# Kernel optimization log

Hardware: AMD Instinct MI355X
Metric: run time of the kernel (lower is better)

Reference implementation:

```python
import jax, jax.numpy as jnp
import numpy as np

N, M, E, DIM, H = 50000, 50000, 640000, 128, 8
DH = DIM // H
EPS = 1e-5

def _prelu(x, alpha):
    return jnp.where(x >= 0, x, alpha * x)

def setup_inputs() -> dict:
    key0 = jax.random.key(0)
    ks = jax.random.split(key0, 12)
    s = 1.0 / np.sqrt(DIM)
    return {
        "query": jax.random.normal(ks[0], (N, DIM), jnp.float32),
        "key": jax.random.normal(ks[1], (M, DIM), jnp.float32),
        "value": jax.random.normal(ks[2], (M, DIM), jnp.float32),
        "query_idx": jax.random.randint(ks[3], (E,), 0, N),
        "key_idx": jax.random.randint(ks[4], (E,), 0, M),
        "Wq": jax.random.normal(ks[5], (DIM, DIM), jnp.float32) * s,
        "bq": jnp.zeros((DIM,), jnp.float32),
        "Wk": jax.random.normal(ks[6], (DIM, DIM), jnp.float32) * s,
        "bk": jnp.zeros((DIM,), jnp.float32),
        "Wv": jax.random.normal(ks[7], (DIM, DIM), jnp.float32) * s,
        "bv": jnp.zeros((DIM,), jnp.float32),
        "Wp": jax.random.normal(ks[8], (DIM, DIM), jnp.float32) * s,
        "bp": jnp.zeros((DIM,), jnp.float32),
        "a": jax.random.normal(ks[9], (1, H, DH), jnp.float32) * 0.1,
        "alpha": jnp.full((1,), 0.25, jnp.float32),
        "gamma": jnp.ones((DIM,), jnp.float32),
        "beta": jnp.zeros((DIM,), jnp.float32),
    }

def reference(query, key, value, query_idx, key_idx, Wq, bq, Wk, bk, Wv, bv, Wp, bp, a, alpha, gamma, beta):
    n = query.shape[0]
    # projections (node-level, then gather per edge; linear commutes with gather)
    Qq = query @ Wq + bq            # [N, DIM]
    Kq = query @ Wk + bk            # [N, DIM] (self-attn key)
    Kk = key @ Wk + bk              # [M, DIM]
    Vq = query @ Wv + bv            # [N, DIM]
    Vv = value @ Wv + bv            # [M, DIM]
    # self-attention score per query node: [N, H, 1]
    attn_qq = (a * _prelu(Qq + Kq, alpha).reshape(n, H, DH)).sum(-1, keepdims=True)
    # per-edge additive attention score: [E, H, 1]
    e_feat = _prelu(Qq[query_idx] + Kk[key_idx], alpha)
    attn_e = (a * e_feat.reshape(-1, H, DH)).sum(-1, keepdims=True)
    # stable softmax over irregular query groups (include self)
    max_attn = jax.lax.stop_gradient(attn_qq.at[query_idx].max(attn_e))
    exp_qq = jnp.exp(attn_qq - max_attn)                 # [N, H, 1]
    exp_e = jnp.exp(attn_e - max_attn[query_idx])        # [E, H, 1]
    denom = exp_qq.at[query_idx].add(exp_e)              # [N, H, 1]
    denom = jnp.where(denom == 0, 1.0, denom)
    # weighted value scatter-sum (value_idx == key_idx)
    msg = exp_qq * Vq.reshape(n, H, DH)
    msg = msg.at[query_idx].add(exp_e * Vv[key_idx].reshape(-1, H, DH))
    out = (msg / denom).reshape(n, DIM) @ Wp + bp
    res = query + out
    mu = res.mean(-1, keepdims=True)
    var = res.var(-1, keepdims=True)
    return gamma * (res - mu) / jnp.sqrt(var + EPS) + beta
```

## Files before the change

kernel.cpp:

```cpp
#include <hip/hip_runtime.h>
#include <math.h>

#define DIM 128
#define NH 8
#define LN_EPS 1e-5f
#define NEGINF -3.0e38f

using bf16x8 = __attribute__((ext_vector_type(8))) short;
using f32x4  = __attribute__((ext_vector_type(4))) float;

__device__ __forceinline__ float prelu_f(float x, float al) { return x >= 0.f ? x : al * x; }

__device__ __forceinline__ short f2bf(float f) {
    unsigned u = __float_as_uint(f);
    unsigned r = (u + 0x7fffu + ((u >> 16) & 1u)) >> 16;
    return (short)r;
}
__device__ __forceinline__ float bflo(unsigned u) { return __uint_as_float(u << 16); }
__device__ __forceinline__ float bfhi(unsigned u) { return __uint_as_float(u & 0xffff0000u); }

__device__ __forceinline__ unsigned cvt_pk_bf16(float lo, float hi) {
    unsigned r;
    asm("v_cvt_pk_bf16_f32 %0, %1, %2" : "=v"(r) : "v"(lo), "v"(hi));
    return r;
}

__device__ __forceinline__ float swz_xor1(float x) {
    return __int_as_float(__builtin_amdgcn_ds_swizzle(__float_as_int(x), 0x041F));
}
__device__ __forceinline__ float swz_xor2(float x) {
    return __int_as_float(__builtin_amdgcn_ds_swizzle(__float_as_int(x), 0x081F));
}
__device__ __forceinline__ float swz_xor4(float x) {
    return __int_as_float(__builtin_amdgcn_ds_swizzle(__float_as_int(x), 0x101F));
}
__device__ __forceinline__ float swz_xor8(float x) {
    return __int_as_float(__builtin_amdgcn_ds_swizzle(__float_as_int(x), 0x201F));
}
__device__ __forceinline__ float swz_xor16(float x) {
    return __int_as_float(__builtin_amdgcn_ds_swizzle(__float_as_int(x), 0x401F));
}
__device__ __forceinline__ float swz_xor32(float x) {
    return __shfl_xor(x, 32);
}

__global__ __launch_bounds__(256) void setup_kernel(
    const float* __restrict__ W0, const float* __restrict__ W1,
    const float* __restrict__ W2, const float* __restrict__ W3,
    short* __restrict__ P0, short* __restrict__ P1,
    short* __restrict__ P2, short* __restrict__ P3,
    const int* __restrict__ qidx, int* __restrict__ counts, int E)
{
    if (blockIdx.x < 32) {
        const int id = blockIdx.x * 256 + threadIdx.x;
        const int mat = id >> 11;
        const int rem = id & 2047;
        const int ks = rem >> 9;
        const int ct = (rem >> 6) & 7;
        const int lane = rem & 63;
        const int lr = lane & 15, lg = lane >> 4;
        const float* W = mat == 0 ? W0 : mat == 1 ? W1 : mat == 2 ? W2 : W3;
        short* P = mat == 0 ? P0 : mat == 1 ? P1 : mat == 2 ? P2 : P3;
        short v[8];
        #pragma unroll
        for (int r = 0; r < 8; ++r)
            v[r] = f2bf(W[(ks * 32 + lg * 8 + r) * DIM + ct * 16 + lr]);
        *(bf16x8*)&P[(size_t)((ks * 8 + ct) * 64 + lane) * 8] = *(bf16x8*)v;
    } else {
        const int b = blockIdx.x - 32;
        for (int e = b * 256 + threadIdx.x; e < E; e += 1024 * 256)
            atomicAdd(&counts[qidx[e]], 1);
    }
}

__global__ __launch_bounds__(256) void proj_all_mfma(
    const float* __restrict__ query,
    const float* __restrict__ key, const float* __restrict__ value,
    const short* __restrict__ Wqp, const short* __restrict__ Wkp, const short* __restrict__ Wvp,
    const float* __restrict__ bq, const float* __restrict__ bk, const float* __restrict__ bv,
    const float* __restrict__ avec, const float* __restrict__ alpha_p,
    short* __restrict__ QV16, float* __restrict__ attnqq,
    short* __restrict__ KV16, int N, int M, int nb)
{
    __shared__ unsigned lds[4][16][66];
    const int wid = threadIdx.x >> 6, lane = threadIdx.x & 63;
    const int lr = lane & 15, lg = lane >> 4;
    const bool evenlane = (lane & 1) == 0;

    if ((int)blockIdx.x < nb) {
        const int row0 = ((int)blockIdx.x * 4 + wid) * 16;
        if (row0 >= N) return;
        const int arow = row0 + lr;
        const bool rowok = arow < N;

        bf16x8 afrag[4];
        #pragma unroll
        for (int ks = 0; ks < 4; ++ks) {
            float t[8] = {0.f,0.f,0.f,0.f,0.f,0.f,0.f,0.f};
            if (rowok) {
                *(float4*)&t[0] = *(const float4*)&query[(size_t)arow * DIM + ks * 32 + lg * 8];
                *(float4*)&t[4] = *(const float4*)&query[(size_t)arow * DIM + ks * 32 + lg * 8 + 4];
            }
            union { bf16x8 v; unsigned u[4]; } a;
            a.u[0] = cvt_pk_bf16(t[0], t[1]);
            a.u[1] = cvt_pk_bf16(t[2], t[3]);
            a.u[2] = cvt_pk_bf16(t[4], t[5]);
            a.u[3] = cvt_pk_bf16(t[6], t[7]);
            afrag[ks] = a.v;
        }
        const float al = alpha_p[0];
        unsigned* qvout = (unsigned*)QV16;

        #pragma unroll 1
        for (int ct = 0; ct < 8; ++ct) {
            f32x4 aq = (f32x4)0.f, ak = (f32x4)0.f;
            #pragma unroll
            for (int ks = 0; ks < 4; ++ks) {
                const size_t bo = (size_t)((ks * 8 + ct) * 64 + lane) * 8;
                aq = __builtin_amdgcn_mfma_f32_16x16x32_bf16(afrag[ks], *(const bf16x8*)&Wqp[bo], aq, 0, 0, 0);
                ak = __builtin_amdgcn_mfma_f32_16x16x32_bf16(afrag[ks], *(const bf16x8*)&Wkp[bo], ak, 0, 0, 0);
            }
            const int col = ct * 16 + lr;
            const float bqv = bq[col], bkv = bk[col], av = avec[col];
            #pragma unroll
            for (int r = 0; r < 4; ++r) {
                const int row = lg * 4 + r;
                const float qv = aq[r] + bqv;
                const float kv = ak[r] + bkv;
                float part = av * prelu_f(qv + kv, al);
                part += swz_xor1(part);
                part += swz_xor2(part);
                part += swz_xor4(part);
                part += swz_xor8(part);
                const int grow = row0 + row;
                if (lr == 0 && grow < N) attnqq[(size_t)grow * NH + ct] = part;
                const float qn = swz_xor1(qv);
                if (evenlane) lds[wid][row][ct * 8 + (lr >> 1)] = cvt_pk_bf16(qv, qn);
            }
        }
        #pragma unroll
        for (int rr = 0; rr < 16; ++rr) {
            const int grow = row0 + rr;
            if (grow < N) qvout[(size_t)grow * 128 + lane] = lds[wid][rr][lane];
        }

        #pragma unroll 1
        for (int ct = 0; ct < 8; ++ct) {
            f32x4 acv = (f32x4)0.f;
            #pragma unroll
            for (int ks = 0; ks < 4; ++ks) {
                const size_t bo = (size_t)((ks * 8 + ct) * 64 + lane) * 8;
                acv = __builtin_amdgcn_mfma_f32_16x16x32_bf16(afrag[ks], *(const bf16x8*)&Wvp[bo], acv, 0, 0, 0);
            }
            const int col = ct * 16 + lr;
            const float bvv = bv[col];
            #pragma unroll
            for (int r = 0; r < 4; ++r) {
                const int row = lg * 4 + r;
                const float vv = acv[r] + bvv;
                const float vn = swz_xor1(vv);
                if (evenlane) lds[wid][row][ct * 8 + (lr >> 1)] = cvt_pk_bf16(vv, vn);
            }
        }
        #pragma unroll
        for (int rr = 0; rr < 16; ++rr) {
            const int grow = row0 + rr;
            if (grow < N) qvout[(size_t)grow * 128 + 64 + lane] = lds[wid][rr][lane];
        }
    } else {
        const int row0 = (((int)blockIdx.x - nb) * 4 + wid) * 16;
        if (row0 >= M) return;
        const int arow = row0 + lr;
        const bool rowok = arow < M;
        unsigned* kvout = (unsigned*)KV16;

        {
            bf16x8 afK[4];
            #pragma unroll
            for (int ks = 0; ks < 4; ++ks) {
                float t[8] = {0.f,0.f,0.f,0.f,0.f,0.f,0.f,0.f};
                if (rowok) {
                    *(float4*)&t[0] = *(const float4*)&key[(size_t)arow * DIM + ks * 32 + lg * 8];
                    *(float4*)&t[4] = *(const float4*)&key[(size_t)arow * DIM + ks * 32 + lg * 8 + 4];
                }
                union { bf16x8 v; unsigned u[4]; } a;
                a.u[0] = cvt_pk_bf16(t[0], t[1]);
                a.u[1] = cvt_pk_bf16(t[2], t[3]);
                a.u[2] = cvt_pk_bf16(t[4], t[5]);
                a.u[3] = cvt_pk_bf16(t[6], t[7]);
                afK[ks] = a.v;
            }
            #pragma unroll 1
            for (int ct = 0; ct < 8; ++ct) {
                f32x4 ack = (f32x4)0.f;
                #pragma unroll
                for (int ks = 0; ks < 4; ++ks) {
                    const size_t bo = (size_t)((ks * 8 + ct) * 64 + lane) * 8;
                    ack = __builtin_amdgcn_mfma_f32_16x16x32_bf16(afK[ks], *(const bf16x8*)&Wkp[bo], ack, 0, 0, 0);
                }
                const int col = ct * 16 + lr;
                const float bkv = bk[col];
                #pragma unroll
                for (int r = 0; r < 4; ++r) {
                    const int row = lg * 4 + r;
                    const float kv = ack[r] + bkv;
                    const float kn = swz_xor1(kv);
                    if (evenlane) lds[wid][row][ct * 8 + (lr >> 1)] = cvt_pk_bf16(kv, kn);
                }
            }
            #pragma unroll
            for (int rr = 0; rr < 16; ++rr) {
                const int grow = row0 + rr;
                if (grow < M) kvout[(size_t)grow * 128 + lane] = lds[wid][rr][lane];
            }
        }
        {
            bf16x8 afV[4];
            #pragma unroll
            for (int ks = 0; ks < 4; ++ks) {
                float t[8] = {0.f,0.f,0.f,0.f,0.f,0.f,0.f,0.f};
                if (rowok) {
                    *(float4*)&t[0] = *(const float4*)&value[(size_t)arow * DIM + ks * 32 + lg * 8];
                    *(float4*)&t[4] = *(const float4*)&value[(size_t)arow * DIM + ks * 32 + lg * 8 + 4];
                }
                union { bf16x8 v; unsigned u[4]; } a;
                a.u[0] = cvt_pk_bf16(t[0], t[1]);
                a.u[1] = cvt_pk_bf16(t[2], t[3]);
                a.u[2] = cvt_pk_bf16(t[4], t[5]);
                a.u[3] = cvt_pk_bf16(t[6], t[7]);
                afV[ks] = a.v;
            }
            #pragma unroll 1
            for (int ct = 0; ct < 8; ++ct) {
                f32x4 acv = (f32x4)0.f;
                #pragma unroll
                for (int ks = 0; ks < 4; ++ks) {
                    const size_t bo = (size_t)((ks * 8 + ct) * 64 + lane) * 8;
                    acv = __builtin_amdgcn_mfma_f32_16x16x32_bf16(afV[ks], *(const bf16x8*)&Wvp[bo], acv, 0, 0, 0);
                }
                const int col = ct * 16 + lr;
                const float bvv = bv[col];
                #pragma unroll
                for (int r = 0; r < 4; ++r) {
                    const int row = lg * 4 + r;
                    const float vv = acv[r] + bvv;
                    const float vn = swz_xor1(vv);
                    if (evenlane) lds[wid][row][ct * 8 + (lr >> 1)] = cvt_pk_bf16(vv, vn);
                }
            }
            #pragma unroll
            for (int rr = 0; rr < 16; ++rr) {
                const int grow = row0 + rr;
                if (grow < M) kvout[(size_t)grow * 128 + 64 + lane] = lds[wid][rr][lane];
            }
        }
    }
}

__global__ __launch_bounds__(256) void scan1_kernel(const int* __restrict__ counts,
                                                    int* __restrict__ bsum, int N)
{
    __shared__ int sh[256];
    int i = blockIdx.x * 256 + threadIdx.x;
    sh[threadIdx.x] = (i < N) ? counts[i] : 0;
    __syncthreads();
    #pragma unroll
    for (int off = 128; off; off >>= 1) {
        if (threadIdx.x < off) sh[threadIdx.x] += sh[threadIdx.x + off];
        __syncthreads();
    }
    if (threadIdx.x == 0) bsum[blockIdx.x] = sh[0];
}

__global__ __launch_bounds__(256) void scan2_kernel(const int* __restrict__ bsum,
                                                    int* __restrict__ boff, int B)
{
    int t = threadIdx.x;
    if (B > 256) {
        if (t == 0) { int run = 0; for (int i = 0; i < B; ++i) { int v = bsum[i]; boff[i] = run; run += v; } }
        return;
    }
    __shared__ int sh[256];
    int v = (t < B) ? bsum[t] : 0;
    sh[t] = v;
    __syncthreads();
    for (int off = 1; off < 256; off <<= 1) {
        int x = (t >= off) ? sh[t - off] : 0;
        __syncthreads();
        sh[t] += x;
        __syncthreads();
    }
    if (t < B) boff[t] = sh[t] - v;
}

__global__ __launch_bounds__(256) void scan3_kernel(const int* __restrict__ counts,
                                                    const int* __restrict__ boff,
                                                    int* __restrict__ offsets,
                                                    int* __restrict__ cursor,
                                                    int N, int E)
{
    __shared__ int sh[256];
    int t = threadIdx.x;
    int i = blockIdx.x * 256 + t;
    int v = (i < N) ? counts[i] : 0;
    sh[t] = v;
    __syncthreads();
    for (int off = 1; off < 256; off <<= 1) {
        int x = (t >= off) ? sh[t - off] : 0;
        __syncthreads();
        sh[t] += x;
        __syncthreads();
    }
    int base = boff[blockIdx.x];
    if (i < N) {
        int o = base + sh[t] - v;
        offsets[i] = o;
        cursor[i] = o;
    }
    if (i == 0) offsets[N] = E;
}

__global__ void fill_kernel(const int* __restrict__ qidx, const int* __restrict__ kidx,
                            int* __restrict__ cursor, int* __restrict__ ksorted, int E)
{
    for (int e = blockIdx.x * blockDim.x + threadIdx.x; e < E; e += gridDim.x * blockDim.x) {
        int q = qidx[e];
        int pos = atomicAdd(&cursor[q], 1);
        ksorted[pos] = kidx[e];
    }
}

__global__ __launch_bounds__(256) void edge_agg_kernel(
    const short* __restrict__ QV16, const float* __restrict__ attnqq,
    const short* __restrict__ KV16,
    const int* __restrict__ ksorted, const int* __restrict__ offsets,
    const float* __restrict__ avec, const float* __restrict__ alpha_p,
    short* __restrict__ msgn16, int N)
{
    const int wid = threadIdx.x >> 6;
    const int lane = threadIdx.x & 63;
    const int n = blockIdx.x * 4 + wid;
    if (n >= N) return;

    const int h = lane & 7;
    const int e = lane >> 3;
    const float al = alpha_p[0];

    float c1[16], c2[16];
    {
        const float s1 = (1.f + al) * 0.5f, s2 = (1.f - al) * 0.5f;
        #pragma unroll
        for (int j = 0; j < 4; ++j) {
            const float4 a4 = *(const float4*)&avec[h * 16 + j * 4];
            c1[j*4+0] = a4.x * s1; c2[j*4+0] = a4.x * s2;
            c1[j*4+1] = a4.y * s1; c2[j*4+1] = a4.y * s2;
            c1[j*4+2] = a4.z * s1; c2[j*4+2] = a4.z * s2;
            c1[j*4+3] = a4.w * s1; c2[j*4+3] = a4.w * s2;
        }
    }

    const size_t qb = (size_t)n * 256 + h * 16;
    float q[16];
    {
        const uint4 lo = *(const uint4*)&QV16[qb];
        const uint4 hi = *(const uint4*)&QV16[qb + 8];
        const unsigned qd[8] = {lo.x, lo.y, lo.z, lo.w, hi.x, hi.y, hi.z, hi.w};
        #pragma unroll
        for (int j = 0; j < 8; ++j) { q[2*j] = bflo(qd[j]); q[2*j+1] = bfhi(qd[j]); }
    }

    float acc[16];
    float den;
    if (e == 0) {
        const uint4 lo = *(const uint4*)&QV16[qb + 128];
        const uint4 hi = *(const uint4*)&QV16[qb + 136];
        const unsigned vd[8] = {lo.x, lo.y, lo.z, lo.w, hi.x, hi.y, hi.z, hi.w};
        #pragma unroll
        for (int j = 0; j < 8; ++j) { acc[2*j] = bflo(vd[j]); acc[2*j+1] = bfhi(vd[j]); }
        den = 1.f;
    } else {
        #pragma unroll
        for (int d = 0; d < 16; ++d) acc[d] = 0.f;
        den = 0.f;
    }

    float m = attnqq[(size_t)n * NH + h];
    const int p0 = offsets[n], p1 = offsets[n + 1];
    bool div = false;

    int idx = p0 + e;
    bool valid = idx < p1;
    int ki = valid ? ksorted[idx] : 0;

    for (int base = p0; base < p1; base += 8) {
        const int cki = ki;
        const bool cval = valid;
        const int nidx = base + 8 + e;
        valid = nidx < p1;
        ki = valid ? ksorted[nidx] : 0;

        const size_t kb = (size_t)cki * 256 + h * 16;
        const uint4 klo = *(const uint4*)&KV16[kb];
        const uint4 khi = *(const uint4*)&KV16[kb + 8];
        const uint4 vlo = *(const uint4*)&KV16[kb + 128];
        const uint4 vhi = *(const uint4*)&KV16[kb + 136];
        const unsigned kd[8] = {klo.x, klo.y, klo.z, klo.w, khi.x, khi.y, khi.z, khi.w};
        const unsigned vd[8] = {vlo.x, vlo.y, vlo.z, vlo.w, vhi.x, vhi.y, vhi.z, vhi.w};

        float sA = 0.f, sB = 0.f;
        #pragma unroll
        for (int j = 0; j < 8; ++j) {
            const float x0 = q[2*j]   + bflo(kd[j]);
            const float x1 = q[2*j+1] + bfhi(kd[j]);
            sA = fmaf(c1[2*j],   x0, fmaf(c2[2*j],   __builtin_fabsf(x0), sA));
            sB = fmaf(c1[2*j+1], x1, fmaf(c2[2*j+1], __builtin_fabsf(x1), sB));
        }
        const float s = cval ? (sA + sB) : NEGINF;
        const float d_ = s - m;

        if (__any(d_ > 8.f)) {
            div = true;
            const float nm = fmaxf(m, s);
            const float c = __expf(m - nm);
            const float w = __expf(s - nm);
            den = den * c + w;
            #pragma unroll
            for (int j = 0; j < 8; ++j) {
                acc[2*j]   = fmaf(acc[2*j],   c, w * bflo(vd[j]));
                acc[2*j+1] = fmaf(acc[2*j+1], c, w * bfhi(vd[j]));
            }
            m = nm;
        } else {
            const float w = __expf(d_);
            den += w;
            #pragma unroll
            for (int j = 0; j < 8; ++j) {
                acc[2*j]   = fmaf(w, bflo(vd[j]), acc[2*j]);
                acc[2*j+1] = fmaf(w, bfhi(vd[j]), acc[2*j+1]);
            }
        }
    }

    #define MERGE_ROUND(SWZ)                                    \
        {                                                       \
            const float m2 = SWZ(m);                            \
            const float den2 = SWZ(den);                        \
            const float nm = fmaxf(m, m2);                      \
            const float ca = __expf(m - nm);                    \
            const float cb = __expf(m2 - nm);                   \
            den = den * ca + den2 * cb;                         \
            _Pragma("unroll")                                   \
            for (int d = 0; d < 16; ++d)                        \
                acc[d] = acc[d] * ca + SWZ(acc[d]) * cb;        \
            m = nm;                                             \
        }
    #define SUM_ROUND(SWZ)                                      \
        {                                                       \
            den += SWZ(den);                                    \
            _Pragma("unroll")                                   \
            for (int d = 0; d < 16; ++d) acc[d] += SWZ(acc[d]); \
        }

    if (div) {
        MERGE_ROUND(swz_xor8);
        MERGE_ROUND(swz_xor16);
        MERGE_ROUND(swz_xor32);
    } else {
        SUM_ROUND(swz_xor8);
        SUM_ROUND(swz_xor16);
        SUM_ROUND(swz_xor32);
    }
    #undef MERGE_ROUND
    #undef SUM_ROUND

    if (e == 0) {
        const float inv = 1.f / den;
        unsigned u[8];
        #pragma unroll
        for (int j = 0; j < 8; ++j)
            u[j] = cvt_pk_bf16(acc[2*j] * inv, acc[2*j+1] * inv);
        *(uint4*)&msgn16[(size_t)n * DIM + h * 16]     = make_uint4(u[0], u[1], u[2], u[3]);
        *(uint4*)&msgn16[(size_t)n * DIM + h * 16 + 8] = make_uint4(u[4], u[5], u[6], u[7]);
    }
}

__global__ __launch_bounds__(256) void out_ln_mfma(
    const short* __restrict__ msgn16, const short* __restrict__ Wpp,
    const float* __restrict__ bp, const float* __restrict__ query,
    const float* __restrict__ gamma, const float* __restrict__ beta,
    float* __restrict__ out, int N)
{
    __shared__ float ys[64][130];
    const int wid = threadIdx.x >> 6, lane = threadIdx.x & 63;
    const int rowbase = blockIdx.x * 64;
    const int row0 = rowbase + wid * 16;
    const int lr = lane & 15, lg = lane >> 4;

    if (row0 < N) {
        bf16x8 afrag[4];
        const int arow = row0 + lr;
        const bool rowok = arow < N;
        #pragma unroll
        for (int ks = 0; ks < 4; ++ks) {
            if (rowok)
                afrag[ks] = *(const bf16x8*)&msgn16[(size_t)arow * DIM + ks * 32 + lg * 8];
            else {
                bf16x8 z;
                #pragma unroll
                for (int j = 0; j < 8; ++j) z[j] = 0;
                afrag[ks] = z;
            }
        }
        #pragma unroll 1
        for (int ct = 0; ct < 8; ++ct) {
            f32x4 acc = (f32x4)0.f;
            #pragma unroll
            for (int ks = 0; ks < 4; ++ks) {
                const size_t bo = (size_t)((ks * 8 + ct) * 64 + lane) * 8;
                acc = __builtin_amdgcn_mfma_f32_16x16x32_bf16(afrag[ks], *(const bf16x8*)&Wpp[bo], acc, 0, 0, 0);
            }
            const int col = ct * 16 + lr;
            const float bpv = bp[col];
            #pragma unroll
            for (int r = 0; r < 4; ++r)
                ys[wid * 16 + lg * 4 + r][col] = acc[r] + bpv;
        }
    }
    __syncthreads();

    for (int rr = 0; rr < 16; ++rr) {
        const int r = wid * 16 + rr;
        const int grow = rowbase + r;
        if (grow >= N) break;
        const float y1 = ys[r][lane], y2 = ys[r][lane + 64];
        const float q1 = query[(size_t)grow * DIM + lane];
        const float q2 = query[(size_t)grow * DIM + lane + 64];
        const float r1 = y1 + q1, r2 = y2 + q2;
        float s = r1 + r2;
        float ss = r1 * r1 + r2 * r2;
        #pragma unroll
        for (int off = 32; off; off >>= 1) {
            s += __shfl_xor(s, off);
            ss += __shfl_xor(ss, off);
        }
        const float mu = s * (1.f / DIM);
        const float var = ss * (1.f / DIM) - mu * mu;
        const float rstd = rsqrtf(var + LN_EPS);
        out[(size_t)grow * DIM + lane] = gamma[lane] * (r1 - mu) * rstd + beta[lane];
        out[(size_t)grow * DIM + lane + 64] = gamma[lane + 64] * (r2 - mu) * rstd + beta[lane + 64];
    }
}

extern "C" void kernel_launch(void* const* d_in, const int* in_sizes, int n_in,
                              void* d_out, int out_size, void* d_ws, size_t ws_size,
                              hipStream_t stream) {
    const float* query = (const float*)d_in[0];
    const float* key   = (const float*)d_in[1];
    const float* value = (const float*)d_in[2];
    const int* query_idx = (const int*)d_in[3];
    const int* key_idx   = (const int*)d_in[4];
    const float* Wq = (const float*)d_in[5];
    const float* bq = (const float*)d_in[6];
    const float* Wk = (const float*)d_in[7];
    const float* bk = (const float*)d_in[8];
    const float* Wv = (const float*)d_in[9];
    const float* bv = (const float*)d_in[10];
    const float* Wp = (const float*)d_in[11];
    const float* bp = (const float*)d_in[12];
    const float* avec  = (const float*)d_in[13];
    const float* alpha = (const float*)d_in[14];
    const float* gamma = (const float*)d_in[15];
    const float* beta  = (const float*)d_in[16];
    float* out = (float*)d_out;

    const int N = in_sizes[0] / DIM;
    const int M = in_sizes[1] / DIM;
    const int E = in_sizes[3];

    float* f = (float*)d_ws;
    float* attnqq = f;  f += (size_t)N * NH;
    short* sp = (short*)f;
    short* QV16 = sp;   sp += (size_t)N * 256;
    short* KV16 = sp;   sp += (size_t)M * 256;
    short* msgn16 = sp; sp += (size_t)N * DIM;
    short* Wqp = sp;    sp += DIM * DIM;
    short* Wkp = sp;    sp += DIM * DIM;
    short* Wvp = sp;    sp += DIM * DIM;
    short* Wpp = sp;    sp += DIM * DIM;
    int* ip = (int*)(((size_t)sp + 15) & ~(size_t)15);
    int* counts  = ip;  ip += N;
    int* offsets = ip;  ip += N + 1;
    int* cursor  = ip;  ip += N;
    int* bsum    = ip;  ip += 4096;
    int* boff    = ip;  ip += 4096;
    int* ksorted = ip;  ip += E;

    const int B = (N + 255) / 256;
    const int nb = (N + 63) / 64;
    const int mb = (M + 63) / 64;

    hipMemsetAsync(counts, 0, (size_t)N * sizeof(int), stream);

    setup_kernel<<<1056, 256, 0, stream>>>(Wq, Wk, Wv, Wp, Wqp, Wkp, Wvp, Wpp,
                                           query_idx, counts, E);

    scan1_kernel<<<B, 256, 0, stream>>>(counts, bsum, N);
    scan2_kernel<<<1, 256, 0, stream>>>(bsum, boff, B);
    scan3_kernel<<<B, 256, 0, stream>>>(counts, boff, offsets, cursor, N, E);
    fill_kernel<<<1024, 256, 0, stream>>>(query_idx, key_idx, cursor, ksorted, E);

    proj_all_mfma<<<nb + mb, 256, 0, stream>>>(
        query, key, value, Wqp, Wkp, Wvp, bq, bk, bv, avec, alpha,
        QV16, attnqq, KV16, N, M, nb);

    edge_agg_kernel<<<(N + 3) / 4, 256, 0, stream>>>(
        QV16, attnqq, KV16, ksorted, offsets, avec, alpha, msgn16, N);

    out_ln_mfma<<<(N + 63) / 64, 256, 0, stream>>>(
        msgn16, Wpp, bp, query, gamma, beta, out, N);
}
```

Before: 206.7 us.

## Remap edge aggregation to two nodes per wave with grid-stride loop

Edge aggregation now gives each wavefront two query nodes instead of one. Each node gets 32 lanes, split into 2 edge slots of 16 lanes, and each lane handles 8 dims, so a head spans a lane pair joined by an xor-1 swizzle. The PReLU dot product is folded into one FMA per element using a precomputed ratio, and the cross-edge merge now needs a single xor-16 swizzle round instead of three. The kernel becomes persistent with a fixed 2048-block grid. Fewer edges are in flight per node per iteration (2 instead of 8), which may increase loop trips for high-degree nodes, in exchange for better lane utilisation and less reduction overhead.

```diff
diff --git a/kernel.cpp b/kernel.cpp
--- a/kernel.cpp
+++ b/kernel.cpp
@@ -39,9 +39,6 @@
 }
 __device__ __forceinline__ float swz_xor16(float x) {
     return __int_as_float(__builtin_amdgcn_ds_swizzle(__float_as_int(x), 0x401F));
-}
-__device__ __forceinline__ float swz_xor32(float x) {
-    return __shfl_xor(x, 32);
 }
 
 __global__ __launch_bounds__(256) void setup_kernel(
@@ -337,150 +334,137 @@
     const float* __restrict__ avec, const float* __restrict__ alpha_p,
     short* __restrict__ msgn16, int N)
 {
-    const int wid = threadIdx.x >> 6;
     const int lane = threadIdx.x & 63;
-    const int n = blockIdx.x * 4 + wid;
-    if (n >= N) return;
-
-    const int h = lane & 7;
-    const int e = lane >> 3;
+    const int wid  = threadIdx.x >> 6;
+    const int half = lane >> 5;
+    const int e    = (lane >> 4) & 1;
+    const int sub  = lane & 15;
+    const int h    = sub >> 1;
+
     const float al = alpha_p[0];
-
-    float c1[16], c2[16];
+    const float r  = (1.f - al) / (1.f + al);
+    const float s1 = (1.f + al) * 0.5f;
+
+    float c[8];
     {
-        const float s1 = (1.f + al) * 0.5f, s2 = (1.f - al) * 0.5f;
-        #pragma unroll
-        for (int j = 0; j < 4; ++j) {
-            const float4 a4 = *(const float4*)&avec[h * 16 + j * 4];
-            c1[j*4+0] = a4.x * s1; c2[j*4+0] = a4.x * s2;
-            c1[j*4+1] = a4.y * s1; c2[j*4+1] = a4.y * s2;
-            c1[j*4+2] = a4.z * s1; c2[j*4+2] = a4.z * s2;
-            c1[j*4+3] = a4.w * s1; c2[j*4+3] = a4.w * s2;
-        }
-    }
-
-    const size_t qb = (size_t)n * 256 + h * 16;
-    float q[16];
-    {
-        const uint4 lo = *(const uint4*)&QV16[qb];
-        const uint4 hi = *(const uint4*)&QV16[qb + 8];
-        const unsigned qd[8] = {lo.x, lo.y, lo.z, lo.w, hi.x, hi.y, hi.z, hi.w};
-        #pragma unroll
-        for (int j = 0; j < 8; ++j) { q[2*j] = bflo(qd[j]); q[2*j+1] = bfhi(qd[j]); }
-    }
-
-    float acc[16];
-    float den;
-    if (e == 0) {
-        const uint4 lo = *(const uint4*)&QV16[qb + 128];
-        const uint4 hi = *(const uint4*)&QV16[qb + 136];
-        const unsigned vd[8] = {lo.x, lo.y, lo.z, lo.w, hi.x, hi.y, hi.z, hi.w};
-        #pragma unroll
-        for (int j = 0; j < 8; ++j) { acc[2*j] = bflo(vd[j]); acc[2*j+1] = bfhi(vd[j]); }
-        den = 1.f;
-    } else {
-        #pragma unroll
-        for (int d = 0; d < 16; ++d) acc[d] = 0.f;
-        den = 0.f;
-    }
-
-    float m = attnqq[(size_t)n * NH + h];
-    const int p0 = offsets[n], p1 = offsets[n + 1];
-    bool div = false;
-
-    int idx = p0 + e;
-    bool valid = idx < p1;
-    int ki = valid ? ksorted[idx] : 0;
-
-    for (int base = p0; base < p1; base += 8) {
-        const int cki = ki;
-        const bool cval = valid;
-        const int nidx = base + 8 + e;
-        valid = nidx < p1;
-        ki = valid ? ksorted[nidx] : 0;
-
-        const size_t kb = (size_t)cki * 256 + h * 16;
-        const uint4 klo = *(const uint4*)&KV16[kb];
-        const uint4 khi = *(const uint4*)&KV16[kb + 8];
-        const uint4 vlo = *(const uint4*)&KV16[kb + 128];
-        const uint4 vhi = *(const uint4*)&KV16[kb + 136];
-        const unsigned kd[8] = {klo.x, klo.y, klo.z, klo.w, khi.x, khi.y, khi.z, khi.w};
-        const unsigned vd[8] = {vlo.x, vlo.y, vlo.z, vlo.w, vhi.x, vhi.y, vhi.z, vhi.w};
-
-        float sA = 0.f, sB = 0.f;
-        #pragma unroll
-        for (int j = 0; j < 8; ++j) {
-            const float x0 = q[2*j]   + bflo(kd[j]);
-            const float x1 = q[2*j+1] + bfhi(kd[j]);
-            sA = fmaf(c1[2*j],   x0, fmaf(c2[2*j],   __builtin_fabsf(x0), sA));
-            sB = fmaf(c1[2*j+1], x1, fmaf(c2[2*j+1], __builtin_fabsf(x1), sB));
-        }
-        const float s = cval ? (sA + sB) : NEGINF;
-        const float d_ = s - m;
-
-        if (__any(d_ > 8.f)) {
-            div = true;
-            const float nm = fmaxf(m, s);
-            const float c = __expf(m - nm);
-            const float w = __expf(s - nm);
-            den = den * c + w;
-            #pragma unroll
-            for (int j = 0; j < 8; ++j) {
-                acc[2*j]   = fmaf(acc[2*j],   c, w * bflo(vd[j]));
-                acc[2*j+1] = fmaf(acc[2*j+1], c, w * bfhi(vd[j]));
-            }
-            m = nm;
+        const float4 a0 = *(const float4*)&avec[sub * 8];
+        const float4 a1 = *(const float4*)&avec[sub * 8 + 4];
+        c[0] = a0.x * s1; c[1] = a0.y * s1; c[2] = a0.z * s1; c[3] = a0.w * s1;
+        c[4] = a1.x * s1; c[5] = a1.y * s1; c[6] = a1.z * s1; c[7] = a1.w * s1;
+    }
+
+    const int npairs = (N + 1) >> 1;
+    const int wavesTotal = gridDim.x * 4;
+
+    for (int pair = blockIdx.x * 4 + wid; pair < npairs; pair += wavesTotal) {
+        const int n = pair * 2 + half;
+        const bool nvalid = n < N;
+        const int nn = nvalid ? n : (N - 1);
+
+        float q[8];
+        {
+            unsigned qd[4];
+            *(uint4*)qd = *(const uint4*)&QV16[(size_t)nn * 256 + sub * 8];
+            #pragma unroll
+            for (int j = 0; j < 4; ++j) { q[2*j] = bflo(qd[j]); q[2*j+1] = bfhi(qd[j]); }
+        }
+
+        float acc[8];
+        float den;
+        if (e == 0) {
+            unsigned vd0[4];
+            *(uint4*)vd0 = *(const uint4*)&QV16[(size_t)nn * 256 + 128 + sub * 8];
+            #pragma unroll
+            for (int j = 0; j < 4; ++j) { acc[2*j] = bflo(vd0[j]); acc[2*j+1] = bfhi(vd0[j]); }
+            den = 1.f;
         } else {
-            const float w = __expf(d_);
-            den += w;
-            #pragma unroll
-            for (int j = 0; j < 8; ++j) {
-                acc[2*j]   = fmaf(w, bflo(vd[j]), acc[2*j]);
-                acc[2*j+1] = fmaf(w, bfhi(vd[j]), acc[2*j+1]);
-            }
-        }
-    }
-
-    #define MERGE_ROUND(SWZ)                                    \
-        {                                                       \
-            const float m2 = SWZ(m);                            \
-            const float den2 = SWZ(den);                        \
-            const float nm = fmaxf(m, m2);                      \
-            const float ca = __expf(m - nm);                    \
-            const float cb = __expf(m2 - nm);                   \
-            den = den * ca + den2 * cb;                         \
-            _Pragma("unroll")                                   \
-            for (int d = 0; d < 16; ++d)                        \
-                acc[d] = acc[d] * ca + SWZ(acc[d]) * cb;        \
-            m = nm;                                             \
-        }
-    #define SUM_ROUND(SWZ)                                      \
-        {                                                       \
-            den += SWZ(den);                                    \
-            _Pragma("unroll")                                   \
-            for (int d = 0; d < 16; ++d) acc[d] += SWZ(acc[d]); \
-        }
-
-    if (div) {
-        MERGE_ROUND(swz_xor8);
-        MERGE_ROUND(swz_xor16);
-        MERGE_ROUND(swz_xor32);
-    } else {
-        SUM_ROUND(swz_xor8);
-        SUM_ROUND(swz_xor16);
-        SUM_ROUND(swz_xor32);
-    }
-    #undef MERGE_ROUND
-    #undef SUM_ROUND
-
-    if (e == 0) {
-        const float inv = 1.f / den;
-        unsigned u[8];
-        #pragma unroll
-        for (int j = 0; j < 8; ++j)
-            u[j] = cvt_pk_bf16(acc[2*j] * inv, acc[2*j+1] * inv);
-        *(uint4*)&msgn16[(size_t)n * DIM + h * 16]     = make_uint4(u[0], u[1], u[2], u[3]);
-        *(uint4*)&msgn16[(size_t)n * DIM + h * 16 + 8] = make_uint4(u[4], u[5], u[6], u[7]);
+            #pragma unroll
+            for (int d = 0; d < 8; ++d) acc[d] = 0.f;
+            den = 0.f;
+        }
+
+        float m = attnqq[(size_t)nn * NH + h];
+        const int p0 = nvalid ? offsets[nn] : 0;
+        const int p1 = nvalid ? offsets[nn + 1] : 0;
+        bool div = false;
+
+        int idx = p0 + e;
+        bool valid = idx < p1;
+        int ki = valid ? ksorted[idx] : 0;
+
+        for (int it = 1; __any(valid); ++it) {
+            const bool cval = valid;
+            const int cki = ki;
+            const int nidx = p0 + it * 2 + e;
+            valid = nidx < p1;
+            ki = valid ? ksorted[nidx] : 0;
+
+            const size_t kb = (size_t)cki * 256 + sub * 8;
+            unsigned kd[4], vd[4];
+            *(uint4*)kd = *(const uint4*)&KV16[kb];
+            *(uint4*)vd = *(const uint4*)&KV16[kb + 128];
+
+            float sp = 0.f;
+            #pragma unroll
+            for (int j = 0; j < 4; ++j) {
+                const float x0 = q[2*j]   + bflo(kd[j]);
+                const float x1 = q[2*j+1] + bfhi(kd[j]);
+                const float t0 = fmaf(r, __builtin_fabsf(x0), x0);
+                const float t1 = fmaf(r, __builtin_fabsf(x1), x1);
+                sp = fmaf(c[2*j], t0, sp);
+                sp = fmaf(c[2*j+1], t1, sp);
+            }
+            const float sf = sp + swz_xor1(sp);
+            const float s = cval ? sf : NEGINF;
+            const float d_ = s - m;
+
+            if (__any(d_ > 8.f)) {
+                div = true;
+                const float nm = fmaxf(m, s);
+                const float cc = __expf(m - nm);
+                const float w = __expf(s - nm);
+                den = den * cc + w;
+                #pragma unroll
+                for (int j = 0; j < 4; ++j) {
+                    acc[2*j]   = fmaf(acc[2*j],   cc, w * bflo(vd[j]));
+                    acc[2*j+1] = fmaf(acc[2*j+1], cc, w * bfhi(vd[j]));
+                }
+                m = nm;
+            } else {
+                const float w = __expf(d_);
+                den += w;
+                #pragma unroll
+                for (int j = 0; j < 4; ++j) {
+                    acc[2*j]   = fmaf(w, bflo(vd[j]), acc[2*j]);
+                    acc[2*j+1] = fmaf(w, bfhi(vd[j]), acc[2*j+1]);
+                }
+            }
+        }
+
+        if (div) {
+            const float m2 = swz_xor16(m);
+            const float den2 = swz_xor16(den);
+            const float nm = fmaxf(m, m2);
+            const float ca = __expf(m - nm);
+            const float cb = __expf(m2 - nm);
+            den = den * ca + den2 * cb;
+            #pragma unroll
+            for (int d = 0; d < 8; ++d)
+                acc[d] = acc[d] * ca + swz_xor16(acc[d]) * cb;
+        } else {
+            den += swz_xor16(den);
+            #pragma unroll
+            for (int d = 0; d < 8; ++d) acc[d] += swz_xor16(acc[d]);
+        }
+
+        if (e == 0 && nvalid) {
+            const float inv = 1.f / den;
+            unsigned u[4];
+            #pragma unroll
+            for (int j = 0; j < 4; ++j)
+                u[j] = cvt_pk_bf16(acc[2*j] * inv, acc[2*j+1] * inv);
+            *(uint4*)&msgn16[(size_t)n * DIM + sub * 8] = *(uint4*)u;
+        }
     }
 }
 
@@ -613,7 +597,7 @@
         query, key, value, Wqp, Wkp, Wvp, bq, bk, bv, avec, alpha,
         QV16, attnqq, KV16, N, M, nb);
 
-    edge_agg_kernel<<<(N + 3) / 4, 256, 0, stream>>>(
+    edge_agg_kernel<<<2048, 256, 0, stream>>>(
         QV16, attnqq, KV16, ksorted, offsets, avec, alpha, msgn16, N);
 
     out_ln_mfma<<<(N + 63) / 64, 256, 0, stream>>>(
```

Result: no change. 208.8 us (+1.0%).
